# Kernel tuning notes

Measured on AMD Instinct MI355X. Metric: run time of the kernel, lower is better.

## Reference

```python
import jax, jax.numpy as jnp
import numpy as np

LN_EPS = 1e-5  # torch nn.LayerNorm default


def setup_inputs() -> dict:
    key = jax.random.key(0)
    ks = jax.random.split(key, 8)
    B, S, H, A, L = 32, 2048, 1024, 256, 10
    return {
        "hidden_states": jax.random.normal(ks[0], (B, S, H), dtype=jnp.float32),
        "language_ids": jax.random.randint(ks[1], (B,), 0, L, dtype=jnp.int64),
        "W1": jax.random.normal(ks[2], (L, H, A), dtype=jnp.float32) * (1.0 / np.sqrt(H)),
        "b1": jnp.zeros((L, A), dtype=jnp.float32),
        "W2": jax.random.normal(ks[3], (L, A, H), dtype=jnp.float32) * (1.0 / np.sqrt(A)),
        "b2": jnp.zeros((L, H), dtype=jnp.float32),
        "gamma": jnp.ones((L, H), dtype=jnp.float32),
        "beta": jnp.zeros((L, H), dtype=jnp.float32),
    }


def reference(hidden_states, language_ids, W1, b1, W2, b2, gamma, beta):
    # Gather each sample's language-specific adapter params: [B, ...]
    w1 = W1[language_ids]                       # [B, H, A]
    w2 = W2[language_ids]                       # [B, A, H]
    # Bottleneck MLP (dropout is identity at inference)
    h = jnp.einsum('bsh,bha->bsa', hidden_states, w1) + b1[language_ids][:, None, :]
    h = jax.nn.relu(h)
    adapted = jnp.einsum('bsa,bah->bsh', h, w2) + b2[language_ids][:, None, :]
    # Residual + per-language LayerNorm over last dim
    x = hidden_states + adapted
    mean = jnp.mean(x, axis=-1, keepdims=True)
    var = jnp.mean(jnp.square(x - mean), axis=-1, keepdims=True)
    normed = (x - mean) * jax.lax.rsqrt(var + LN_EPS)
    return normed * gamma[language_ids][:, None, :] + beta[language_ids][:, None, :]
```

## Files before the change

kernel.cpp:

```cpp
#include <hip/hip_runtime.h>

#define B_  32
#define S_  2048
#define H_  1024
#define A_  256
#define L_  10

typedef unsigned short u16;
typedef _Float16 f16;
typedef f16   f16v8 __attribute__((ext_vector_type(8)));
typedef float f32x4 __attribute__((ext_vector_type(4)));

typedef __attribute__((address_space(1))) const unsigned int gu32_t;
typedef __attribute__((address_space(3))) unsigned int lu32_t;
__device__ __forceinline__ void glds16(const void* g, void* l) {
    __builtin_amdgcn_global_load_lds((gu32_t*)g, (lu32_t*)l, 16, 0, 0);
}

__global__ __launch_bounds__(256) void pack_weights(
    const float* __restrict__ W1, const float* __restrict__ W2,
    f16* __restrict__ w1p, f16* __restrict__ w2p)
{
    const int p = blockIdx.x;
    const int t = threadIdx.x;
    const float* src; int sstride; f16* dst; size_t dbase;
    if (p < 320) {
        int lid = p >> 5, ktg = p & 31;
        src = W1 + ((size_t)lid * H_ + ktg * 32) * A_;
        sstride = A_;
        dst = w1p; dbase = (size_t)(lid * 32 + ktg) * 8192;
    } else {
        int p2 = p - 320;
        int lid = p2 >> 5, kt = (p2 >> 2) & 7, nq = p2 & 3;
        src = W2 + ((size_t)lid * A_ + kt * 32) * H_ + nq * 256;
        sstride = H_;
        dst = w2p; dbase = ((size_t)(lid * 8 + kt) * 64 + nq * 16) * 512;
    }
    const int ln = t & 63;
    const int k0 = (ln >> 4) * 8;
    const int nn = ln & 15;
    #pragma unroll
    for (int r = 0; r < 4; ++r) {
        int nt = r * 4 + (t >> 6);
        const float* s = src + (size_t)k0 * sstride + nt * 16 + nn;
        f16v8 h8;
        #pragma unroll
        for (int i = 0; i < 8; ++i) h8[i] = (f16)s[(size_t)i * sstride];
        *(f16v8*)(dst + dbase + (size_t)nt * 512 + (size_t)ln * 8) = h8;
    }
}

__global__ __launch_bounds__(512, 4) void fused_adapter(
    const float* __restrict__ X, const int* __restrict__ langs,
    const float* __restrict__ b1, const float* __restrict__ b2,
    const float* __restrict__ gamma, const float* __restrict__ beta,
    const f16* __restrict__ w1p, const f16* __restrict__ w2p,
    float* __restrict__ out)
{
    __shared__ f16   hh[32 * 256];
    __shared__ f16   xbuf[2][32][40];
    __shared__ f16   wbuf[2][16 * 512];
    __shared__ float part[32][4][2];
    __shared__ float mrstd[32][2];

    const int fid = blockIdx.x;
    const int uu  = fid >> 3;
    const int b   = (fid & 7) * 4 + (uu >> 6);
    const int s0  = (uu & 63) * 32;
    const int lid = langs[b];

    const int t = threadIdx.x, lane = t & 63, wid = t >> 6;
    const int wm = wid >> 2, wn = wid & 3;
    const int lr = lane & 15, lg = lane >> 4;

    const float* Xb = X + ((size_t)(b * S_ + s0)) * H_;
    const f16* w1base = w1p + (size_t)lid * 32 * 8192;
    const f16* w2base = w2p + (size_t)lid * 8 * 64 * 512;

    f32x4 acc1[4];
    #pragma unroll
    for (int nf = 0; nf < 4; ++nf) acc1[nf] = f32x4{0.f, 0.f, 0.f, 0.f};

    const int srow = t >> 4, skk = (t & 15) * 2;

    float2 xheld;
    {
        #pragma unroll
        for (int j = 0; j < 2; ++j)
            glds16(w1base + (size_t)(0 * 16 + wid * 2 + j) * 512 + lane * 8,
                   &wbuf[0][(wid * 2 + j) * 512]);
        float2 x0 = *(const float2*)(Xb + (size_t)srow * H_ + skk);
        xbuf[0][srow][skk]     = (f16)x0.x;
        xbuf[0][srow][skk + 1] = (f16)x0.y;
        xheld = *(const float2*)(Xb + (size_t)srow * H_ + 32 + skk);
    }
    __syncthreads();

    #pragma unroll 1
    for (int kt = 0; kt < 32; ++kt) {
        const int cur = kt & 1, nxt = cur ^ 1;
        if (kt < 31) {
            #pragma unroll
            for (int j = 0; j < 2; ++j)
                glds16(w1base + ((size_t)(kt + 1) * 16 + wid * 2 + j) * 512 + lane * 8,
                       &wbuf[nxt][(wid * 2 + j) * 512]);
        }
        float2 xnew;
        if (kt < 30)
            xnew = *(const float2*)(Xb + (size_t)srow * H_ + (kt + 2) * 32 + skk);

        const int arow = wm * 16 + lr;
        f16v8 a = *(const f16v8*)&xbuf[cur][arow][lg * 8];
        #pragma unroll
        for (int nf = 0; nf < 4; ++nf) {
            f16v8 bb = *(const f16v8*)&wbuf[cur][(wn * 4 + nf) * 512 + lane * 8];
            acc1[nf] = __builtin_amdgcn_mfma_f32_16x16x32_f16(a, bb, acc1[nf], 0, 0, 0);
        }
        if (kt < 31) {
            xbuf[nxt][srow][skk]     = (f16)xheld.x;
            xbuf[nxt][srow][skk + 1] = (f16)xheld.y;
        }
        xheld = xnew;
        __syncthreads();
    }

    #pragma unroll
    for (int nf = 0; nf < 4; ++nf) {
        int k = wn * 64 + nf * 16 + lr;
        float bias = b1[lid * A_ + k];
        #pragma unroll
        for (int r = 0; r < 4; ++r) {
            int row = wm * 16 + lg * 4 + r;
            float v = acc1[nf][r] + bias;
            v = v > 0.f ? v : 0.f;
            hh[row * 256 + (k ^ ((row & 7) << 3))] = (f16)v;
        }
    }
    __syncthreads();
    #pragma unroll
    for (int j = 0; j < 2; ++j)
        glds16(w2base + (size_t)(0 * 64 + 0 * 16 + wid * 2 + j) * 512 + lane * 8,
               &wbuf[0][(wid * 2 + j) * 512]);
    __syncthreads();

    f32x4 acc2[16];
    #pragma unroll
    for (int i = 0; i < 16; ++i) acc2[i] = f32x4{0.f, 0.f, 0.f, 0.f};

    #pragma unroll 1
    for (int kt = 0; kt < 8; ++kt) {
        const int arow = wm * 16 + lr;
        f16v8 a2 = *(const f16v8*)&hh[arow * 256 + ((kt * 32 + lg * 8) ^ ((arow & 7) << 3))];
        #pragma unroll
        for (int q = 0; q < 4; ++q) {
            const int ph = kt * 4 + q, cur = q & 1, nxt = cur ^ 1;
            if (ph < 31) {
                int pn = ph + 1, kn = pn >> 2, qn = pn & 3;
                #pragma unroll
                for (int j = 0; j < 2; ++j)
                    glds16(w2base + ((size_t)kn * 64 + qn * 16 + wid * 2 + j) * 512 + lane * 8,
                           &wbuf[nxt][(wid * 2 + j) * 512]);
            }
            #pragma unroll
            for (int nf = 0; nf < 4; ++nf) {
                f16v8 bb = *(const f16v8*)&wbuf[cur][(wn * 4 + nf) * 512 + lane * 8];
                acc2[q * 4 + nf] = __builtin_amdgcn_mfma_f32_16x16x32_f16(a2, bb, acc2[q * 4 + nf], 0, 0, 0);
            }
            __syncthreads();
        }
    }

    float s1[4], s2[4];
    #pragma unroll
    for (int r = 0; r < 4; ++r) { s1[r] = 0.f; s2[r] = 0.f; }

    #pragma unroll
    for (int q = 0; q < 4; ++q)
        #pragma unroll
        for (int nf = 0; nf < 4; ++nf) {
            int col = (q * 16 + wn * 4 + nf) * 16 + lr;
            float bb = b2[lid * H_ + col];
            #pragma unroll
            for (int r = 0; r < 4; ++r) {
                int row = wm * 16 + lg * 4 + r;
                float x = acc2[q * 4 + nf][r] + bb + Xb[(size_t)row * H_ + col];
                acc2[q * 4 + nf][r] = x;
                s1[r] += x; s2[r] += x * x;
            }
        }

    #pragma unroll
    for (int r = 0; r < 4; ++r) {
        float a = s1[r], c = s2[r];
        #pragma unroll
        for (int m = 1; m < 16; m <<= 1) { a += __shfl_xor(a, m); c += __shfl_xor(c, m); }
        if (lr == 0) {
            int row = wm * 16 + lg * 4 + r;
            part[row][wn][0] = a; part[row][wn][1] = c;
        }
    }
    __syncthreads();
    if (t < 32) {
        float a = part[t][0][0] + part[t][1][0] + part[t][2][0] + part[t][3][0];
        float c = part[t][0][1] + part[t][1][1] + part[t][2][1] + part[t][3][1];
        float mean = a * (1.f / 1024.f);
        float var  = c * (1.f / 1024.f) - mean * mean;
        mrstd[t][0] = mean;
        mrstd[t][1] = rsqrtf(var + 1e-5f);
    }
    __syncthreads();

    float* ob = out + ((size_t)(b * S_ + s0)) * H_;
    #pragma unroll
    for (int q = 0; q < 4; ++q)
        #pragma unroll
        for (int nf = 0; nf < 4; ++nf) {
            int col = (q * 16 + wn * 4 + nf) * 16 + lr;
            float g  = gamma[lid * H_ + col];
            float bt = beta[lid * H_ + col];
            #pragma unroll
            for (int r = 0; r < 4; ++r) {
                int row = wm * 16 + lg * 4 + r;
                float x = acc2[q * 4 + nf][r];
                ob[(size_t)row * H_ + col] = (x - mrstd[row][0]) * mrstd[row][1] * g + bt;
            }
        }
}

extern "C" void kernel_launch(void* const* d_in, const int* in_sizes, int n_in,
                              void* d_out, int out_size, void* d_ws, size_t ws_size,
                              hipStream_t stream)
{
    const float* X     = (const float*)d_in[0];
    const int*   langs = (const int*)  d_in[1];
    const float* W1    = (const float*)d_in[2];
    const float* b1    = (const float*)d_in[3];
    const float* W2    = (const float*)d_in[4];
    const float* b2    = (const float*)d_in[5];
    const float* gamma = (const float*)d_in[6];
    const float* beta  = (const float*)d_in[7];
    float* out = (float*)d_out;

    char* ws = (char*)d_ws;
    f16* w1p = (f16*)(ws);
    f16* w2p = (f16*)(ws + 5242880);

    hipLaunchKernelGGL(pack_weights, dim3(640), dim3(256), 0, stream,
                       W1, W2, w1p, w2p);
    hipLaunchKernelGGL(fused_adapter, dim3(2048), dim3(512), 0, stream,
                       X, langs, b1, b2, gamma, beta, w1p, w2p, out);
}
```

Before: 709.4 us.

## Read packed weights directly from global memory and widen X staging chunks

Removes the LDS double-buffering of packed weight tiles (global_load_lds) and has each wave load its MFMA B-fragments straight from global or L2. X is staged in wider 128-column chunks with vectorized float4 loads and swizzled f16 stores, which cuts the number of barriers in GEMM1 from 32 to 8. GEMM2 now needs no barriers, and each wave owns a contiguous 256-column slab. The risk is higher global or L2 traffic and latency exposure on weight loads, since nothing in the code prefetches them, and it relies on the weights staying cache-resident.

```diff
diff --git a/kernel.cpp b/kernel.cpp
--- a/kernel.cpp
+++ b/kernel.cpp
@@ -6,16 +6,9 @@
 #define A_  256
 #define L_  10
 
-typedef unsigned short u16;
 typedef _Float16 f16;
 typedef f16   f16v8 __attribute__((ext_vector_type(8)));
 typedef float f32x4 __attribute__((ext_vector_type(4)));
-
-typedef __attribute__((address_space(1))) const unsigned int gu32_t;
-typedef __attribute__((address_space(3))) unsigned int lu32_t;
-__device__ __forceinline__ void glds16(const void* g, void* l) {
-    __builtin_amdgcn_global_load_lds((gu32_t*)g, (lu32_t*)l, 16, 0, 0);
-}
 
 __global__ __launch_bounds__(256) void pack_weights(
     const float* __restrict__ W1, const float* __restrict__ W2,
@@ -57,9 +50,8 @@
     const f16* __restrict__ w1p, const f16* __restrict__ w2p,
     float* __restrict__ out)
 {
-    __shared__ f16   hh[32 * 256];
-    __shared__ f16   xbuf[2][32][40];
-    __shared__ f16   wbuf[2][16 * 512];
+    __shared__ __align__(16) f16 xbuf[2][32][128];
+    __shared__ __align__(16) f16 hh[32 * 256];
     __shared__ float part[32][4][2];
     __shared__ float mrstd[32][2];
 
@@ -74,53 +66,57 @@
     const int lr = lane & 15, lg = lane >> 4;
 
     const float* Xb = X + ((size_t)(b * S_ + s0)) * H_;
-    const f16* w1base = w1p + (size_t)lid * 32 * 8192;
-    const f16* w2base = w2p + (size_t)lid * 8 * 64 * 512;
+    const f16* w1base = w1p + (size_t)lid * 262144;
+    const f16* w2base = w2p + (size_t)lid * 262144;
 
     f32x4 acc1[4];
     #pragma unroll
     for (int nf = 0; nf < 4; ++nf) acc1[nf] = f32x4{0.f, 0.f, 0.f, 0.f};
 
-    const int srow = t >> 4, skk = (t & 15) * 2;
-
-    float2 xheld;
+    const int srow = t >> 4, scg = (t & 15) * 8;
+    const int sws  = (srow & 7) << 3;
+    f16* xdst0 = &xbuf[0][srow][scg ^ sws];
+    f16* xdst1 = &xbuf[1][srow][scg ^ sws];
+    const float* xsrc = Xb + (size_t)srow * H_ + scg;
+
+    float4 h0, h1;
     {
-        #pragma unroll
-        for (int j = 0; j < 2; ++j)
-            glds16(w1base + (size_t)(0 * 16 + wid * 2 + j) * 512 + lane * 8,
-                   &wbuf[0][(wid * 2 + j) * 512]);
-        float2 x0 = *(const float2*)(Xb + (size_t)srow * H_ + skk);
-        xbuf[0][srow][skk]     = (f16)x0.x;
-        xbuf[0][srow][skk + 1] = (f16)x0.y;
-        xheld = *(const float2*)(Xb + (size_t)srow * H_ + 32 + skk);
+        float4 a0 = *(const float4*)(xsrc);
+        float4 a1 = *(const float4*)(xsrc + 4);
+        f16v8 v = {(f16)a0.x,(f16)a0.y,(f16)a0.z,(f16)a0.w,
+                   (f16)a1.x,(f16)a1.y,(f16)a1.z,(f16)a1.w};
+        *(f16v8*)xdst0 = v;
+        h0 = *(const float4*)(xsrc + 128);
+        h1 = *(const float4*)(xsrc + 132);
     }
     __syncthreads();
 
     #pragma unroll 1
-    for (int kt = 0; kt < 32; ++kt) {
-        const int cur = kt & 1, nxt = cur ^ 1;
-        if (kt < 31) {
+    for (int kc = 0; kc < 8; ++kc) {
+        float4 n0, n1;
+        if (kc < 6) {
+            n0 = *(const float4*)(xsrc + (size_t)(kc + 2) * 128);
+            n1 = *(const float4*)(xsrc + (size_t)(kc + 2) * 128 + 4);
+        }
+        const int arow = wm * 16 + lr;
+        const int swa  = (arow & 7) << 3;
+        #pragma unroll
+        for (int kt = 0; kt < 4; ++kt) {
+            f16v8 a = *(const f16v8*)&xbuf[kc & 1][arow][(kt * 32 + lg * 8) ^ swa];
+            const int kg = kc * 4 + kt;
             #pragma unroll
-            for (int j = 0; j < 2; ++j)
-                glds16(w1base + ((size_t)(kt + 1) * 16 + wid * 2 + j) * 512 + lane * 8,
-                       &wbuf[nxt][(wid * 2 + j) * 512]);
-        }
-        float2 xnew;
-        if (kt < 30)
-            xnew = *(const float2*)(Xb + (size_t)srow * H_ + (kt + 2) * 32 + skk);
-
-        const int arow = wm * 16 + lr;
-        f16v8 a = *(const f16v8*)&xbuf[cur][arow][lg * 8];
-        #pragma unroll
-        for (int nf = 0; nf < 4; ++nf) {
-            f16v8 bb = *(const f16v8*)&wbuf[cur][(wn * 4 + nf) * 512 + lane * 8];
-            acc1[nf] = __builtin_amdgcn_mfma_f32_16x16x32_f16(a, bb, acc1[nf], 0, 0, 0);
-        }
-        if (kt < 31) {
-            xbuf[nxt][srow][skk]     = (f16)xheld.x;
-            xbuf[nxt][srow][skk + 1] = (f16)xheld.y;
-        }
-        xheld = xnew;
+            for (int nf = 0; nf < 4; ++nf) {
+                f16v8 bb = *(const f16v8*)(w1base
+                           + ((size_t)(kg * 16 + wn * 4 + nf)) * 512 + lane * 8);
+                acc1[nf] = __builtin_amdgcn_mfma_f32_16x16x32_f16(a, bb, acc1[nf], 0, 0, 0);
+            }
+        }
+        if (kc < 7) {
+            f16v8 v = {(f16)h0.x,(f16)h0.y,(f16)h0.z,(f16)h0.w,
+                       (f16)h1.x,(f16)h1.y,(f16)h1.z,(f16)h1.w};
+            *(f16v8*)((kc & 1) ? xdst0 : xdst1) = v;
+        }
+        h0 = n0; h1 = n1;
         __syncthreads();
     }
 
@@ -137,57 +133,39 @@
         }
     }
     __syncthreads();
-    #pragma unroll
-    for (int j = 0; j < 2; ++j)
-        glds16(w2base + (size_t)(0 * 64 + 0 * 16 + wid * 2 + j) * 512 + lane * 8,
-               &wbuf[0][(wid * 2 + j) * 512]);
-    __syncthreads();
 
     f32x4 acc2[16];
     #pragma unroll
     for (int i = 0; i < 16; ++i) acc2[i] = f32x4{0.f, 0.f, 0.f, 0.f};
 
-    #pragma unroll 1
-    for (int kt = 0; kt < 8; ++kt) {
+    {
         const int arow = wm * 16 + lr;
-        f16v8 a2 = *(const f16v8*)&hh[arow * 256 + ((kt * 32 + lg * 8) ^ ((arow & 7) << 3))];
-        #pragma unroll
-        for (int q = 0; q < 4; ++q) {
-            const int ph = kt * 4 + q, cur = q & 1, nxt = cur ^ 1;
-            if (ph < 31) {
-                int pn = ph + 1, kn = pn >> 2, qn = pn & 3;
-                #pragma unroll
-                for (int j = 0; j < 2; ++j)
-                    glds16(w2base + ((size_t)kn * 64 + qn * 16 + wid * 2 + j) * 512 + lane * 8,
-                           &wbuf[nxt][(wid * 2 + j) * 512]);
+        const int swa  = (arow & 7) << 3;
+        #pragma unroll 1
+        for (int kt = 0; kt < 8; ++kt) {
+            f16v8 a2 = *(const f16v8*)&hh[arow * 256 + ((kt * 32 + lg * 8) ^ swa)];
+            #pragma unroll
+            for (int nf = 0; nf < 16; ++nf) {
+                f16v8 bb = *(const f16v8*)(w2base
+                           + ((size_t)(kt * 64 + wn * 16 + nf)) * 512 + lane * 8);
+                acc2[nf] = __builtin_amdgcn_mfma_f32_16x16x32_f16(a2, bb, acc2[nf], 0, 0, 0);
             }
-            #pragma unroll
-            for (int nf = 0; nf < 4; ++nf) {
-                f16v8 bb = *(const f16v8*)&wbuf[cur][(wn * 4 + nf) * 512 + lane * 8];
-                acc2[q * 4 + nf] = __builtin_amdgcn_mfma_f32_16x16x32_f16(a2, bb, acc2[q * 4 + nf], 0, 0, 0);
-            }
-            __syncthreads();
-        }
-    }
-
-    float s1[4], s2[4];
-    #pragma unroll
-    for (int r = 0; r < 4; ++r) { s1[r] = 0.f; s2[r] = 0.f; }
-
-    #pragma unroll
-    for (int q = 0; q < 4; ++q)
-        #pragma unroll
-        for (int nf = 0; nf < 4; ++nf) {
-            int col = (q * 16 + wn * 4 + nf) * 16 + lr;
-            float bb = b2[lid * H_ + col];
-            #pragma unroll
-            for (int r = 0; r < 4; ++r) {
-                int row = wm * 16 + lg * 4 + r;
-                float x = acc2[q * 4 + nf][r] + bb + Xb[(size_t)row * H_ + col];
-                acc2[q * 4 + nf][r] = x;
-                s1[r] += x; s2[r] += x * x;
-            }
-        }
+        }
+    }
+
+    float s1[4] = {0.f,0.f,0.f,0.f}, s2[4] = {0.f,0.f,0.f,0.f};
+    #pragma unroll 4
+    for (int nf = 0; nf < 16; ++nf) {
+        int col = wn * 256 + nf * 16 + lr;
+        float bb2 = b2[lid * H_ + col];
+        #pragma unroll
+        for (int r = 0; r < 4; ++r) {
+            int row = wm * 16 + lg * 4 + r;
+            float x = acc2[nf][r] + bb2 + Xb[(size_t)row * H_ + col];
+            acc2[nf][r] = x;
+            s1[r] += x; s2[r] += x * x;
+        }
+    }
 
     #pragma unroll
     for (int r = 0; r < 4; ++r) {
@@ -211,20 +189,18 @@
     __syncthreads();
 
     float* ob = out + ((size_t)(b * S_ + s0)) * H_;
-    #pragma unroll
-    for (int q = 0; q < 4; ++q)
-        #pragma unroll
-        for (int nf = 0; nf < 4; ++nf) {
-            int col = (q * 16 + wn * 4 + nf) * 16 + lr;
-            float g  = gamma[lid * H_ + col];
-            float bt = beta[lid * H_ + col];
-            #pragma unroll
-            for (int r = 0; r < 4; ++r) {
-                int row = wm * 16 + lg * 4 + r;
-                float x = acc2[q * 4 + nf][r];
-                ob[(size_t)row * H_ + col] = (x - mrstd[row][0]) * mrstd[row][1] * g + bt;
-            }
-        }
+    #pragma unroll 4
+    for (int nf = 0; nf < 16; ++nf) {
+        int col = wn * 256 + nf * 16 + lr;
+        float g  = gamma[lid * H_ + col];
+        float bt = beta[lid * H_ + col];
+        #pragma unroll
+        for (int r = 0; r < 4; ++r) {
+            int row = wm * 16 + lg * 4 + r;
+            float x = acc2[nf][r];
+            ob[(size_t)row * H_ + col] = (x - mrstd[row][0]) * mrstd[row][1] * g + bt;
+        }
+    }
 }
 
 extern "C" void kernel_launch(void* const* d_in, const int* in_sizes, int n_in,
```

Measured after the change: 831.4 us. 17.2% more time.
